# Performance work log

Measured on AMD Instinct MI355X. Metric: run time of the kernel, lower is better.

Reference implementation:

```python
import jax, jax.numpy as jnp
import numpy as np

D = 120
H = 8
HD = D // H
LN_EPS = 1e-5


def setup_inputs() -> dict:
    key = jax.random.key(0)
    ks = jax.random.split(key, 8)
    B, N = 16, 8192
    s = 1.0 / np.sqrt(D)
    return {
        "voxel_feat": jax.random.normal(ks[0], (B, N, D), dtype=jnp.float32),
        "cnn_feat": jax.random.normal(ks[1], (B, N, D), dtype=jnp.float32),
        "in_proj_w": jax.random.uniform(ks[2], (3 * D, D), minval=-s, maxval=s, dtype=jnp.float32),
        "in_proj_b": jnp.zeros((3 * D,), dtype=jnp.float32),
        "out_w": jax.random.uniform(ks[3], (D, D), minval=-s, maxval=s, dtype=jnp.float32),
        "out_b": jnp.zeros((D,), dtype=jnp.float32),
        "ln_gamma": jnp.ones((D,), dtype=jnp.float32),
        "ln_beta": jnp.zeros((D,), dtype=jnp.float32),
    }


def reference(voxel_feat, cnn_feat, in_proj_w, in_proj_b, out_w, out_b, ln_gamma, ln_beta):
    B, N, _ = voxel_feat.shape
    # (B, N, 2, D) -> (B*N, 2, D): each location is a 2-token sequence
    x = jnp.stack([voxel_feat, cnn_feat], axis=2).reshape(B * N, 2, D)
    # fused QKV projection (torch in_proj): x @ W^T + b
    qkv = x @ in_proj_w.T + in_proj_b                      # (BN, 2, 3D)
    q, k, v = jnp.split(qkv, 3, axis=-1)                   # each (BN, 2, D)
    # split heads: (BN, 2, H, HD) -> (BN, H, 2, HD)
    def heads(t):
        return t.reshape(B * N, 2, H, HD).transpose(0, 2, 1, 3)
    q, k, v = heads(q), heads(k), heads(v)
    scale = 1.0 / np.sqrt(HD)
    scores = jnp.einsum('bhqd,bhkd->bhqk', q, k) * scale   # (BN, H, 2, 2)
    attn = jax.nn.softmax(scores, axis=-1)
    o = jnp.einsum('bhqk,bhkd->bhqd', attn, v)             # (BN, H, 2, HD)
    o = o.transpose(0, 2, 1, 3).reshape(B * N, 2, D)
    y = o @ out_w.T + out_b                                # output projection
    # layernorm over last dim (eps = torch default 1e-5)
    mu = y.mean(axis=-1, keepdims=True)
    var = ((y - mu) ** 2).mean(axis=-1, keepdims=True)
    y = (y - mu) * jax.lax.rsqrt(var + LN_EPS) * ln_gamma + ln_beta
    # mean-pool the 2 tokens
    fused = y.mean(axis=1).reshape(B, N, D)
    return fused
```

## Files before the change

### kernel.cpp

```cpp
#include <hip/hip_runtime.h>
#include <hip/hip_bf16.h>
#include <stdint.h>

#define DD 120
#define HD 15
#define LN_EPS 1e-5f

typedef __attribute__((ext_vector_type(8))) short bf16x8;
typedef __attribute__((ext_vector_type(4))) float f32x4;

__device__ __forceinline__ unsigned short f2bf(float f) {
    return __bfloat16_as_ushort(__float2bfloat16(f));
}

__global__ void prep_weights(const float* __restrict__ w1, const float* __restrict__ w2,
                             const float* __restrict__ b1, const float* __restrict__ b2,
                             unsigned short* __restrict__ W1bp, unsigned short* __restrict__ W2bp) {
    int idx = blockIdx.x * blockDim.x + threadIdx.x;
    int stride = gridDim.x * blockDim.x;
    for (int p = idx; p < 24 * 4 * 64 * 8; p += stride) {
        int e = p & 7, lane = (p >> 3) & 63, kk = (p >> 9) & 3, t = p >> 11;
        int pos = t * 16 + (lane & 15);
        int part = pos >> 7, rem = pos & 127, h = rem >> 4, i = rem & 15;
        int k = kk * 32 + (lane >> 4) * 8 + e;
        float v = 0.f;
        if (k < DD)        { if (i < HD) v = w1[(part * DD + h * HD + i) * DD + k]; }
        else if (k == DD)  { if (i < HD) v = b1[part * DD + h * HD + i];
                             else if (part == 2 && h == 0) v = 1.0f; }
        W1bp[p] = f2bf(v);
    }
    for (int p = idx; p < 8 * 4 * 64 * 8; p += stride) {
        int e = p & 7, lane = (p >> 3) & 63, kk = (p >> 9) & 3, t = p >> 11;
        int n = t * 16 + (lane & 15);
        int kpad = kk * 32 + (lane >> 4) * 8 + e;
        int i = kpad & 15;
        int h = kpad >> 4;
        float v = 0.f;
        if (n < DD) {
            if (i < HD) v = w2[n * DD + h * HD + i];
            else if (kpad == 15) v = b2[n];
        }
        W2bp[p] = f2bf(v);
    }
}

__global__ __launch_bounds__(256, 3) void fused_attn(
    const float* __restrict__ voxel, const float* __restrict__ cnnf,
    const float* __restrict__ gamma, const float* __restrict__ beta,
    const unsigned short* __restrict__ W1bp, const unsigned short* __restrict__ W2bp,
    float* __restrict__ out)
{
    __shared__ __align__(16) char smem[49152];
    unsigned short* xs   = (unsigned short*)smem;
    unsigned short* obuf = (unsigned short*)(smem + 32768);
    float* yf = (float*)smem;

    const int tid = threadIdx.x;
    const int wave = tid >> 6, lane = tid & 63;
    const int lrow = lane & 15, lk = lane >> 4;
    const int w = wave;
    const int r7 = lrow & 7;
    const int tok0 = blockIdx.x * 64;

    bf16x8 A[2][4];
    #pragma unroll
    for (int kk = 0; kk < 4; ++kk) {
        A[0][kk] = *(const bf16x8*)(W1bp + ((size_t)(((0 * 8 + w) * 4 + kk) * 64 + lane)) * 8);
        A[1][kk] = *(const bf16x8*)(W1bp + ((size_t)(((1 * 8 + w) * 4 + kk) * 64 + lane)) * 8);
    }

    #pragma unroll
    for (int j = 0; j < 8; ++j) {
        int i = tid + j * 256;
        int r = i >> 5, c4 = i & 31;
        ushort4 hv;
        if (c4 < 30) {
            int gtok = tok0 + r;
            const float* src = ((gtok & 1) ? cnnf : voxel) + (size_t)(gtok >> 1) * DD + c4 * 4;
            float4 f = *(const float4*)src;
            hv.x = f2bf(f.x); hv.y = f2bf(f.y); hv.z = f2bf(f.z); hv.w = f2bf(f.w);
        } else if (c4 == 30) {
            hv.x = 0x3F80; hv.y = 0; hv.z = 0; hv.w = 0;
        } else {
            hv.x = 0; hv.y = 0; hv.z = 0; hv.w = 0;
        }
        int c8 = c4 >> 1, sub = (c4 & 1) * 8;
        *(ushort4*)((char*)xs + r * 256 + ((c8 ^ (r & 7)) << 4) + sub) = hv;
    }
    __syncthreads();

    bf16x8 bfr[4][4];
    #pragma unroll
    for (int b = 0; b < 4; ++b)
        #pragma unroll
        for (int kk = 0; kk < 4; ++kk) {
            int chunk = kk * 4 + lk;
            bfr[b][kk] = *(const bf16x8*)((const char*)xs + (b * 16 + lrow) * 256 + ((chunk ^ r7) << 4));
        }

    const float scale = 0.25819888974716112567f;
    #pragma unroll
    for (int hh = 0; hh < 2; ++hh) {
        int h = w + 4 * hh;
        f32x4 acc[3][4];
        __builtin_amdgcn_s_setprio(1);
        #pragma unroll
        for (int part = 0; part < 3; ++part) {
            int u = hh * 3 + part;
            #pragma unroll
            for (int b = 0; b < 4; ++b) {
                f32x4 a = {0.f, 0.f, 0.f, 0.f};
                #pragma unroll
                for (int kk = 0; kk < 4; ++kk)
                    a = __builtin_amdgcn_mfma_f32_16x16x32_bf16(A[u & 1][kk], bfr[b][kk], a, 0, 0, 0);
                acc[part][b] = a;
            }
            if (u + 2 < 6) {
                int v = u + 2;
                int t2 = (v % 3) * 8 + (w + 4 * (v / 3));
                #pragma unroll
                for (int kk = 0; kk < 4; ++kk)
                    A[u & 1][kk] = *(const bf16x8*)(W1bp + ((size_t)((t2 * 4 + kk) * 64 + lane)) * 8);
            }
        }
        __builtin_amdgcn_s_setprio(0);
        #pragma unroll
        for (int b = 0; b < 4; ++b) {
            f32x4 Q = acc[0][b], K = acc[1][b], V = acc[2][b];
            float kn0 = __shfl_xor(K[0], 1), kn1 = __shfl_xor(K[1], 1);
            float kn2 = __shfl_xor(K[2], 1), kn3 = __shfl_xor(K[3], 1);
            float ps = Q[0] * K[0] + Q[1] * K[1] + Q[2] * K[2] + Q[3] * K[3];
            float pn = Q[0] * kn0 + Q[1] * kn1 + Q[2] * kn2 + Q[3] * kn3;
            ps += __shfl_xor(ps, 16); ps += __shfl_xor(ps, 32);
            pn += __shfl_xor(pn, 16); pn += __shfl_xor(pn, 32);
            float d = (pn - ps) * scale;
            float p0 = 1.f / (1.f + __expf(d));
            float p1 = 1.f - p0;
            float o0 = p0 * V[0] + p1 * __shfl_xor(V[0], 1);
            float o1 = p0 * V[1] + p1 * __shfl_xor(V[1], 1);
            float o2 = p0 * V[2] + p1 * __shfl_xor(V[2], 1);
            float o3 = p0 * V[3] + p1 * __shfl_xor(V[3], 1);
            unsigned w0 = (unsigned)f2bf(o0) | ((unsigned)f2bf(o1) << 16);
            unsigned w1v = (unsigned)f2bf(o2) | ((unsigned)f2bf(o3) << 16);
            int chunk = 2 * h + (lk >> 1);
            *(uint2*)((char*)obuf + (b * 16 + lrow) * 256 + ((chunk ^ r7) << 4) + (lk & 1) * 8)
                = make_uint2(w0, w1v);
        }
    }

    bf16x8 A2[2][4];
    #pragma unroll
    for (int ti = 0; ti < 2; ++ti)
        #pragma unroll
        for (int kk = 0; kk < 4; ++kk)
            A2[ti][kk] = *(const bf16x8*)(W2bp + ((size_t)(((w + 4 * ti) * 4 + kk) * 64 + lane)) * 8);
    __syncthreads();

    {
        bf16x8 ofr[4][4];
        #pragma unroll
        for (int b = 0; b < 4; ++b)
            #pragma unroll
            for (int kk = 0; kk < 4; ++kk) {
                int chunk = kk * 4 + lk;
                ofr[b][kk] = *(const bf16x8*)((const char*)obuf + (b * 16 + lrow) * 256 + ((chunk ^ r7) << 4));
            }
        __builtin_amdgcn_s_setprio(1);
        #pragma unroll
        for (int ti = 0; ti < 2; ++ti) {
            int t = w + 4 * ti;
            int chunk = 4 * t + lk;
            #pragma unroll
            for (int b = 0; b < 4; ++b) {
                f32x4 a = {0.f, 0.f, 0.f, 0.f};
                #pragma unroll
                for (int kk = 0; kk < 4; ++kk)
                    a = __builtin_amdgcn_mfma_f32_16x16x32_bf16(A2[ti][kk], ofr[b][kk], a, 0, 0, 0);
                int row = b * 16 + lrow;
                *(f32x4*)((char*)yf + row * 512 + ((chunk ^ r7) << 4)) = a;
            }
        }
        __builtin_amdgcn_s_setprio(0);
    }
    __syncthreads();

    {
        int locl = tid >> 3;
        int s = tid & 7;
        int r0 = 2 * locl, r1 = r0 + 1;
        auto rdf = [&](int r, int c) -> f32x4 {
            return *(const f32x4*)((const char*)yf + r * 512 + ((c ^ (r & 7)) << 4));
        };
        f32x4 v00 = rdf(r0, 2 * s),      v01 = rdf(r0, 2 * s + 1);
        f32x4 v02 = rdf(r0, 16 + 2 * s), v03 = rdf(r0, 16 + 2 * s + 1);
        f32x4 v10 = rdf(r1, 2 * s),      v11 = rdf(r1, 2 * s + 1);
        f32x4 v12 = rdf(r1, 16 + 2 * s), v13 = rdf(r1, 16 + 2 * s + 1);
        float a0[16], a1[16];
        #pragma unroll
        for (int j = 0; j < 4; ++j) {
            a0[j] = v00[j]; a0[4 + j] = v01[j]; a0[8 + j] = v02[j]; a0[12 + j] = v03[j];
            a1[j] = v10[j]; a1[4 + j] = v11[j]; a1[8 + j] = v12[j]; a1[12 + j] = v13[j];
        }
        float sum0 = 0.f, sq0 = 0.f, sum1 = 0.f, sq1 = 0.f;
        #pragma unroll
        for (int j = 0; j < 16; ++j) {
            sum0 += a0[j]; sq0 += a0[j] * a0[j];
            sum1 += a1[j]; sq1 += a1[j] * a1[j];
        }
        #pragma unroll
        for (int ww = 1; ww < 8; ww <<= 1) {
            sum0 += __shfl_xor(sum0, ww); sq0 += __shfl_xor(sq0, ww);
            sum1 += __shfl_xor(sum1, ww); sq1 += __shfl_xor(sq1, ww);
        }
        const float inv = 1.f / 120.f;
        float mu0 = sum0 * inv, mu1 = sum1 * inv;
        float var0 = sq0 * inv - mu0 * mu0, var1 = sq1 * inv - mu1 * mu1;
        float rs0 = rsqrtf(var0 + LN_EPS), rs1 = rsqrtf(var1 + LN_EPS);
        float* op = out + (size_t)(blockIdx.x * 32 + locl) * DD;
        {
            int c = 8 * s;
            #pragma unroll
            for (int q = 0; q < 2; ++q) {
                f32x4 gm = *(const f32x4*)(gamma + c + 4 * q);
                f32x4 bt = *(const f32x4*)(beta + c + 4 * q);
                float4 o4;
                float z0, z1;
                z0 = (a0[4 * q + 0] - mu0) * rs0; z1 = (a1[4 * q + 0] - mu1) * rs1;
                o4.x = 0.5f * (z0 + z1) * gm[0] + bt[0];
                z0 = (a0[4 * q + 1] - mu0) * rs0; z1 = (a1[4 * q + 1] - mu1) * rs1;
                o4.y = 0.5f * (z0 + z1) * gm[1] + bt[1];
                z0 = (a0[4 * q + 2] - mu0) * rs0; z1 = (a1[4 * q + 2] - mu1) * rs1;
                o4.z = 0.5f * (z0 + z1) * gm[2] + bt[2];
                z0 = (a0[4 * q + 3] - mu0) * rs0; z1 = (a1[4 * q + 3] - mu1) * rs1;
                o4.w = 0.5f * (z0 + z1) * gm[3] + bt[3];
                *(float4*)(op + c + 4 * q) = o4;
            }
        }
        if (s < 7) {
            int c = 64 + 8 * s;
            #pragma unroll
            for (int q = 0; q < 2; ++q) {
                f32x4 gm = *(const f32x4*)(gamma + c + 4 * q);
                f32x4 bt = *(const f32x4*)(beta + c + 4 * q);
                float4 o4;
                float z0, z1;
                z0 = (a0[8 + 4 * q + 0] - mu0) * rs0; z1 = (a1[8 + 4 * q + 0] - mu1) * rs1;
                o4.x = 0.5f * (z0 + z1) * gm[0] + bt[0];
                z0 = (a0[8 + 4 * q + 1] - mu0) * rs0; z1 = (a1[8 + 4 * q + 1] - mu1) * rs1;
                o4.y = 0.5f * (z0 + z1) * gm[1] + bt[1];
                z0 = (a0[8 + 4 * q + 2] - mu0) * rs0; z1 = (a1[8 + 4 * q + 2] - mu1) * rs1;
                o4.z = 0.5f * (z0 + z1) * gm[2] + bt[2];
                z0 = (a0[8 + 4 * q + 3] - mu0) * rs0; z1 = (a1[8 + 4 * q + 3] - mu1) * rs1;
                o4.w = 0.5f * (z0 + z1) * gm[3] + bt[3];
                *(float4*)(op + c + 4 * q) = o4;
            }
        }
    }
}

extern "C" void kernel_launch(void* const* d_in, const int* in_sizes, int n_in,
                              void* d_out, int out_size, void* d_ws, size_t ws_size,
                              hipStream_t stream) {
    const float* voxel = (const float*)d_in[0];
    const float* cnnf  = (const float*)d_in[1];
    const float* w1    = (const float*)d_in[2];
    const float* b1    = (const float*)d_in[3];
    const float* w2    = (const float*)d_in[4];
    const float* b2    = (const float*)d_in[5];
    const float* gamma = (const float*)d_in[6];
    const float* beta  = (const float*)d_in[7];
    float* out = (float*)d_out;

    unsigned short* W1bp = (unsigned short*)d_ws;
    unsigned short* W2bp = (unsigned short*)((char*)d_ws + 98304);

    int nloc = in_sizes[0] / DD;
    prep_weights<<<128, 256, 0, stream>>>(w1, w2, b1, b2, W1bp, W2bp);
    fused_attn<<<nloc / 32, 256, 0, stream>>>(voxel, cnnf, gamma, beta, W1bp, W2bp, out);
}
```

Before: 83.15 us.

## Split fused attention kernel into QKV-attention and projection-layernorm kernels

Replaces the single fused kernel with two kernels: one computes the QKV projection and the 2-token attention and writes bf16 attention outputs to a workspace buffer, and a second reads them back to run the output projection and layernorm with mean pooling. The idea is to cut per-kernel register and shared-memory pressure (16KB and 48KB instead of 48KB with a 3-blocks occupancy cap) so more waves stay resident. In exchange it adds a global round trip of about 64MB of bf16 intermediate data plus an extra launch. The old fused path is kept as a fallback when the workspace is too small.

```diff
diff --git a/kernel.cpp b/kernel.cpp
--- a/kernel.cpp
+++ b/kernel.cpp
@@ -44,6 +44,242 @@
     }
 }
 
+__global__ __launch_bounds__(256) void qkv_attn(
+    const float* __restrict__ voxel, const float* __restrict__ cnnf,
+    const unsigned short* __restrict__ W1bp,
+    unsigned short* __restrict__ Obuf)
+{
+    __shared__ __align__(16) char smem[16384];
+    unsigned short* xs = (unsigned short*)smem;
+
+    const int tid = threadIdx.x;
+    const int wave = tid >> 6, lane = tid & 63;
+    const int lrow = lane & 15, lk = lane >> 4;
+    const int w = wave;
+    const int r7 = lrow & 7;
+    const int tok0 = blockIdx.x * 64;
+
+    bf16x8 A[2][4];
+    #pragma unroll
+    for (int kk = 0; kk < 4; ++kk) {
+        A[0][kk] = *(const bf16x8*)(W1bp + ((size_t)(((0 * 8 + w) * 4 + kk) * 64 + lane)) * 8);
+        A[1][kk] = *(const bf16x8*)(W1bp + ((size_t)(((1 * 8 + w) * 4 + kk) * 64 + lane)) * 8);
+    }
+
+    #pragma unroll
+    for (int j = 0; j < 8; ++j) {
+        int i = tid + j * 256;
+        int r = i >> 5, c4 = i & 31;
+        ushort4 hv;
+        if (c4 < 30) {
+            int gtok = tok0 + r;
+            const float* src = ((gtok & 1) ? cnnf : voxel) + (size_t)(gtok >> 1) * DD + c4 * 4;
+            float4 f = *(const float4*)src;
+            hv.x = f2bf(f.x); hv.y = f2bf(f.y); hv.z = f2bf(f.z); hv.w = f2bf(f.w);
+        } else if (c4 == 30) {
+            hv.x = 0x3F80; hv.y = 0; hv.z = 0; hv.w = 0;
+        } else {
+            hv.x = 0; hv.y = 0; hv.z = 0; hv.w = 0;
+        }
+        int c8 = c4 >> 1, sub = (c4 & 1) * 8;
+        *(ushort4*)((char*)xs + r * 256 + ((c8 ^ (r & 7)) << 4) + sub) = hv;
+    }
+    __syncthreads();
+
+    bf16x8 bfr[4][4];
+    #pragma unroll
+    for (int b = 0; b < 4; ++b)
+        #pragma unroll
+        for (int kk = 0; kk < 4; ++kk) {
+            int chunk = kk * 4 + lk;
+            bfr[b][kk] = *(const bf16x8*)((const char*)xs + (b * 16 + lrow) * 256 + ((chunk ^ r7) << 4));
+        }
+
+    const float scale = 0.25819888974716112567f;
+    #pragma unroll
+    for (int hh = 0; hh < 2; ++hh) {
+        int h = w + 4 * hh;
+        f32x4 acc[3][4];
+        __builtin_amdgcn_s_setprio(1);
+        #pragma unroll
+        for (int part = 0; part < 3; ++part) {
+            int u = hh * 3 + part;
+            #pragma unroll
+            for (int b = 0; b < 4; ++b) {
+                f32x4 a = {0.f, 0.f, 0.f, 0.f};
+                #pragma unroll
+                for (int kk = 0; kk < 4; ++kk)
+                    a = __builtin_amdgcn_mfma_f32_16x16x32_bf16(A[u & 1][kk], bfr[b][kk], a, 0, 0, 0);
+                acc[part][b] = a;
+            }
+            if (u + 2 < 6) {
+                int v = u + 2;
+                int t2 = (v % 3) * 8 + (w + 4 * (v / 3));
+                #pragma unroll
+                for (int kk = 0; kk < 4; ++kk)
+                    A[u & 1][kk] = *(const bf16x8*)(W1bp + ((size_t)((t2 * 4 + kk) * 64 + lane)) * 8);
+            }
+        }
+        __builtin_amdgcn_s_setprio(0);
+        #pragma unroll
+        for (int b = 0; b < 4; ++b) {
+            f32x4 Q = acc[0][b], K = acc[1][b], V = acc[2][b];
+            float kn0 = __shfl_xor(K[0], 1), kn1 = __shfl_xor(K[1], 1);
+            float kn2 = __shfl_xor(K[2], 1), kn3 = __shfl_xor(K[3], 1);
+            float ps = Q[0] * K[0] + Q[1] * K[1] + Q[2] * K[2] + Q[3] * K[3];
+            float pn = Q[0] * kn0 + Q[1] * kn1 + Q[2] * kn2 + Q[3] * kn3;
+            ps += __shfl_xor(ps, 16); ps += __shfl_xor(ps, 32);
+            pn += __shfl_xor(pn, 16); pn += __shfl_xor(pn, 32);
+            float d = (pn - ps) * scale;
+            float p0 = 1.f / (1.f + __expf(d));
+            float p1 = 1.f - p0;
+            float o0 = p0 * V[0] + p1 * __shfl_xor(V[0], 1);
+            float o1 = p0 * V[1] + p1 * __shfl_xor(V[1], 1);
+            float o2 = p0 * V[2] + p1 * __shfl_xor(V[2], 1);
+            float o3 = p0 * V[3] + p1 * __shfl_xor(V[3], 1);
+            unsigned w0 = (unsigned)f2bf(o0) | ((unsigned)f2bf(o1) << 16);
+            unsigned w1v = (unsigned)f2bf(o2) | ((unsigned)f2bf(o3) << 16);
+            int gtok = tok0 + b * 16 + lrow;
+            int chunk = 2 * h + (lk >> 1);
+            *(uint2*)((char*)Obuf + (size_t)gtok * 256 + chunk * 16 + (lk & 1) * 8)
+                = make_uint2(w0, w1v);
+        }
+    }
+}
+
+__global__ __launch_bounds__(256) void proj_ln(
+    const float* __restrict__ gamma, const float* __restrict__ beta,
+    const unsigned short* __restrict__ W2bp,
+    const unsigned short* __restrict__ Obuf,
+    float* __restrict__ out)
+{
+    __shared__ __align__(16) char smem[49152];
+    unsigned short* os = (unsigned short*)smem;
+    float* yf = (float*)(smem + 16384);
+
+    const int tid = threadIdx.x;
+    const int wave = tid >> 6, lane = tid & 63;
+    const int lrow = lane & 15, lk = lane >> 4;
+    const int w = wave;
+    const int r7 = lrow & 7;
+    const int tok0 = blockIdx.x * 64;
+
+    bf16x8 A2[2][4];
+    #pragma unroll
+    for (int ti = 0; ti < 2; ++ti)
+        #pragma unroll
+        for (int kk = 0; kk < 4; ++kk)
+            A2[ti][kk] = *(const bf16x8*)(W2bp + ((size_t)(((w + 4 * ti) * 4 + kk) * 64 + lane)) * 8);
+
+    #pragma unroll
+    for (int j = 0; j < 4; ++j) {
+        int i = tid + j * 256;
+        int r = i >> 4, c = i & 15;
+        uint4 v = *(const uint4*)((const char*)Obuf + (size_t)(tok0 + r) * 256 + c * 16);
+        *(uint4*)((char*)os + r * 256 + ((c ^ (r & 7)) << 4)) = v;
+    }
+    __syncthreads();
+
+    {
+        bf16x8 ofr[4][4];
+        #pragma unroll
+        for (int b = 0; b < 4; ++b)
+            #pragma unroll
+            for (int kk = 0; kk < 4; ++kk) {
+                int chunk = kk * 4 + lk;
+                ofr[b][kk] = *(const bf16x8*)((const char*)os + (b * 16 + lrow) * 256 + ((chunk ^ r7) << 4));
+            }
+        __builtin_amdgcn_s_setprio(1);
+        #pragma unroll
+        for (int ti = 0; ti < 2; ++ti) {
+            int t = w + 4 * ti;
+            int chunk = 4 * t + lk;
+            #pragma unroll
+            for (int b = 0; b < 4; ++b) {
+                f32x4 a = {0.f, 0.f, 0.f, 0.f};
+                #pragma unroll
+                for (int kk = 0; kk < 4; ++kk)
+                    a = __builtin_amdgcn_mfma_f32_16x16x32_bf16(A2[ti][kk], ofr[b][kk], a, 0, 0, 0);
+                int row = b * 16 + lrow;
+                *(f32x4*)((char*)yf + row * 512 + ((chunk ^ r7) << 4)) = a;
+            }
+        }
+        __builtin_amdgcn_s_setprio(0);
+    }
+    __syncthreads();
+
+    {
+        int locl = tid >> 3;
+        int s = tid & 7;
+        int r0 = 2 * locl, r1 = r0 + 1;
+        auto rdf = [&](int r, int c) -> f32x4 {
+            return *(const f32x4*)((const char*)yf + r * 512 + ((c ^ (r & 7)) << 4));
+        };
+        f32x4 v00 = rdf(r0, 2 * s),      v01 = rdf(r0, 2 * s + 1);
+        f32x4 v02 = rdf(r0, 16 + 2 * s), v03 = rdf(r0, 16 + 2 * s + 1);
+        f32x4 v10 = rdf(r1, 2 * s),      v11 = rdf(r1, 2 * s + 1);
+        f32x4 v12 = rdf(r1, 16 + 2 * s), v13 = rdf(r1, 16 + 2 * s + 1);
+        float a0[16], a1[16];
+        #pragma unroll
+        for (int j = 0; j < 4; ++j) {
+            a0[j] = v00[j]; a0[4 + j] = v01[j]; a0[8 + j] = v02[j]; a0[12 + j] = v03[j];
+            a1[j] = v10[j]; a1[4 + j] = v11[j]; a1[8 + j] = v12[j]; a1[12 + j] = v13[j];
+        }
+        float sum0 = 0.f, sq0 = 0.f, sum1 = 0.f, sq1 = 0.f;
+        #pragma unroll
+        for (int j = 0; j < 16; ++j) {
+            sum0 += a0[j]; sq0 += a0[j] * a0[j];
+            sum1 += a1[j]; sq1 += a1[j] * a1[j];
+        }
+        #pragma unroll
+        for (int ww = 1; ww < 8; ww <<= 1) {
+            sum0 += __shfl_xor(sum0, ww); sq0 += __shfl_xor(sq0, ww);
+            sum1 += __shfl_xor(sum1, ww); sq1 += __shfl_xor(sq1, ww);
+        }
+        const float inv = 1.f / 120.f;
+        float mu0 = sum0 * inv, mu1 = sum1 * inv;
+        float var0 = sq0 * inv - mu0 * mu0, var1 = sq1 * inv - mu1 * mu1;
+        float rs0 = rsqrtf(var0 + LN_EPS), rs1 = rsqrtf(var1 + LN_EPS);
+        float* op = out + (size_t)(blockIdx.x * 32 + locl) * DD;
+        {
+            int c = 8 * s;
+            #pragma unroll
+            for (int q = 0; q < 2; ++q) {
+                f32x4 gm = *(const f32x4*)(gamma + c + 4 * q);
+                f32x4 bt = *(const f32x4*)(beta + c + 4 * q);
+                float4 o4; float z0, z1;
+                z0 = (a0[4 * q + 0] - mu0) * rs0; z1 = (a1[4 * q + 0] - mu1) * rs1;
+                o4.x = 0.5f * (z0 + z1) * gm[0] + bt[0];
+                z0 = (a0[4 * q + 1] - mu0) * rs0; z1 = (a1[4 * q + 1] - mu1) * rs1;
+                o4.y = 0.5f * (z0 + z1) * gm[1] + bt[1];
+                z0 = (a0[4 * q + 2] - mu0) * rs0; z1 = (a1[4 * q + 2] - mu1) * rs1;
+                o4.z = 0.5f * (z0 + z1) * gm[2] + bt[2];
+                z0 = (a0[4 * q + 3] - mu0) * rs0; z1 = (a1[4 * q + 3] - mu1) * rs1;
+                o4.w = 0.5f * (z0 + z1) * gm[3] + bt[3];
+                *(float4*)(op + c + 4 * q) = o4;
+            }
+        }
+        if (s < 7) {
+            int c = 64 + 8 * s;
+            #pragma unroll
+            for (int q = 0; q < 2; ++q) {
+                f32x4 gm = *(const f32x4*)(gamma + c + 4 * q);
+                f32x4 bt = *(const f32x4*)(beta + c + 4 * q);
+                float4 o4; float z0, z1;
+                z0 = (a0[8 + 4 * q + 0] - mu0) * rs0; z1 = (a1[8 + 4 * q + 0] - mu1) * rs1;
+                o4.x = 0.5f * (z0 + z1) * gm[0] + bt[0];
+                z0 = (a0[8 + 4 * q + 1] - mu0) * rs0; z1 = (a1[8 + 4 * q + 1] - mu1) * rs1;
+                o4.y = 0.5f * (z0 + z1) * gm[1] + bt[1];
+                z0 = (a0[8 + 4 * q + 2] - mu0) * rs0; z1 = (a1[8 + 4 * q + 2] - mu1) * rs1;
+                o4.z = 0.5f * (z0 + z1) * gm[2] + bt[2];
+                z0 = (a0[8 + 4 * q + 3] - mu0) * rs0; z1 = (a1[8 + 4 * q + 3] - mu1) * rs1;
+                o4.w = 0.5f * (z0 + z1) * gm[3] + bt[3];
+                *(float4*)(op + c + 4 * q) = o4;
+            }
+        }
+    }
+}
+
 __global__ __launch_bounds__(256, 3) void fused_attn(
     const float* __restrict__ voxel, const float* __restrict__ cnnf,
     const float* __restrict__ gamma, const float* __restrict__ beta,
@@ -68,7 +304,6 @@
         A[0][kk] = *(const bf16x8*)(W1bp + ((size_t)(((0 * 8 + w) * 4 + kk) * 64 + lane)) * 8);
         A[1][kk] = *(const bf16x8*)(W1bp + ((size_t)(((1 * 8 + w) * 4 + kk) * 64 + lane)) * 8);
     }
-
     #pragma unroll
     for (int j = 0; j < 8; ++j) {
         int i = tid + j * 256;
@@ -223,8 +458,7 @@
             for (int q = 0; q < 2; ++q) {
                 f32x4 gm = *(const f32x4*)(gamma + c + 4 * q);
                 f32x4 bt = *(const f32x4*)(beta + c + 4 * q);
-                float4 o4;
-                float z0, z1;
+                float4 o4; float z0, z1;
                 z0 = (a0[4 * q + 0] - mu0) * rs0; z1 = (a1[4 * q + 0] - mu1) * rs1;
                 o4.x = 0.5f * (z0 + z1) * gm[0] + bt[0];
                 z0 = (a0[4 * q + 1] - mu0) * rs0; z1 = (a1[4 * q + 1] - mu1) * rs1;
@@ -242,8 +476,7 @@
             for (int q = 0; q < 2; ++q) {
                 f32x4 gm = *(const f32x4*)(gamma + c + 4 * q);
                 f32x4 bt = *(const f32x4*)(beta + c + 4 * q);
-                float4 o4;
-                float z0, z1;
+                float4 o4; float z0, z1;
                 z0 = (a0[8 + 4 * q + 0] - mu0) * rs0; z1 = (a1[8 + 4 * q + 0] - mu1) * rs1;
                 o4.x = 0.5f * (z0 + z1) * gm[0] + bt[0];
                 z0 = (a0[8 + 4 * q + 1] - mu0) * rs0; z1 = (a1[8 + 4 * q + 1] - mu1) * rs1;
@@ -275,6 +508,15 @@
     unsigned short* W2bp = (unsigned short*)((char*)d_ws + 98304);
 
     int nloc = in_sizes[0] / DD;
+    int ntok = nloc * 2;
+    size_t obytes = (size_t)ntok * 128 * 2;
     prep_weights<<<128, 256, 0, stream>>>(w1, w2, b1, b2, W1bp, W2bp);
-    fused_attn<<<nloc / 32, 256, 0, stream>>>(voxel, cnnf, gamma, beta, W1bp, W2bp, out);
+
+    if (ws_size >= (size_t)131072 + obytes) {
+        unsigned short* Obuf = (unsigned short*)((char*)d_ws + 131072);
+        qkv_attn<<<nloc / 32, 256, 0, stream>>>(voxel, cnnf, W1bp, Obuf);
+        proj_ln<<<nloc / 32, 256, 0, stream>>>(gamma, beta, W2bp, Obuf, out);
+    } else {
+        fused_attn<<<nloc / 32, 256, 0, stream>>>(voxel, cnnf, gamma, beta, W1bp, W2bp, out);
+    }
 }
```

Measured after the change: 101.4 us. +22.0%, slower.
